# Kernel tuning notes

Measured on AMD Instinct MI355X. Metric: run time of the kernel, lower is better.

## Reference

```python
import jax, jax.numpy as jnp
import numpy as np

N_NODES = 100000
N_EDGES = 1600000
D = 128


def sage_conv(x, src, dst, W_l, b_l, W_r):
    # mean aggregation of neighbor features: messages flow src -> dst
    msgs = x[src]                                           # [E, D] gather
    agg = jax.ops.segment_sum(msgs, dst, num_segments=x.shape[0])  # [N, D]
    deg = jax.ops.segment_sum(jnp.ones((src.shape[0],), x.dtype), dst,
                              num_segments=x.shape[0])       # [N]
    agg = agg / jnp.maximum(deg, 1.0)[:, None]
    # PyG SAGEConv: lin_l(aggregated) + lin_r(root); bias lives in lin_l
    return agg @ W_l.T + b_l + x @ W_r.T


def setup_inputs() -> dict:
    key = jax.random.key(0)
    ks = jax.random.split(key, 8)
    s = 1.0 / np.sqrt(D)
    return {
        "x": jax.random.normal(ks[0], (N_NODES, D), dtype=jnp.float32),
        "edge_index": jax.random.randint(ks[1], (2, N_EDGES), 0, N_NODES, dtype=jnp.int64),
        "W1_l": jax.random.normal(ks[2], (D, D), dtype=jnp.float32) * s,
        "b1": jnp.zeros((D,), dtype=jnp.float32),
        "W1_r": jax.random.normal(ks[3], (D, D), dtype=jnp.float32) * s,
        "W2_l": jax.random.normal(ks[4], (D, D), dtype=jnp.float32) * s,
        "b2": jnp.zeros((D,), dtype=jnp.float32),
        "W2_r": jax.random.normal(ks[5], (D, D), dtype=jnp.float32) * s,
    }


def reference(x, edge_index, W1_l, b1, W1_r, W2_l, b2, W2_r):
    src, dst = edge_index[0], edge_index[1]
    h = jax.nn.relu(sage_conv(x, src, dst, W1_l, b1, W1_r))
    out = sage_conv(h, src, dst, W2_l, b2, W2_r)
    return out
```

## Files before the change

### kernel.cpp

```cpp
#include <hip/hip_runtime.h>
#include <cstdint>
#include <cstddef>

#define D 128

typedef unsigned short ushort_t;
typedef unsigned int uint_t;
typedef __attribute__((ext_vector_type(8))) short bf16x8;
typedef __attribute__((ext_vector_type(4))) float f32x4;

static __device__ __forceinline__ unsigned short f2bf(float f) {
    unsigned int u = __float_as_uint(f);
    u = (u + 0x7FFFu + ((u >> 16) & 1u)) >> 16;
    return (unsigned short)u;
}
static __device__ __forceinline__ float bf_lo(uint_t v) {
    return __uint_as_float(v << 16);
}
static __device__ __forceinline__ float bf_hi(uint_t v) {
    return __uint_as_float(v & 0xFFFF0000u);
}

static __device__ __forceinline__ void cast8(const float* __restrict__ s,
                                             ushort_t* __restrict__ d) {
    float4 a = *(const float4*)s;
    float4 b = *(const float4*)(s + 4);
    uint4 o;
    o.x = (uint_t)f2bf(a.x) | ((uint_t)f2bf(a.y) << 16);
    o.y = (uint_t)f2bf(a.z) | ((uint_t)f2bf(a.w) << 16);
    o.z = (uint_t)f2bf(b.x) | ((uint_t)f2bf(b.y) << 16);
    o.w = (uint_t)f2bf(b.z) | ((uint_t)f2bf(b.w) << 16);
    *(uint4*)d = o;
}


__global__ __launch_bounds__(256) void front_fused(
    const int* __restrict__ dst, int* __restrict__ bhist, int E, int EB,
    const float* __restrict__ x, ushort_t* __restrict__ xb, long nx, int CX,
    const float* __restrict__ W1l, const float* __restrict__ W1r,
    const float* __restrict__ W2l, const float* __restrict__ W2r,
    ushort_t* __restrict__ W1lb, ushort_t* __restrict__ W1rb,
    ushort_t* __restrict__ W2lb, ushort_t* __restrict__ W2rb,
    int* __restrict__ row_ptr, int N) {
    __shared__ int lh[512];
    int b = blockIdx.x, t = threadIdx.x;
    if (b == 0 && t == 0) row_ptr[N] = E;
    if (b < EB) {
        lh[t] = 0;
        lh[t + 256] = 0;
        __syncthreads();
        int base = b * 4096;
#pragma unroll
        for (int i = 0; i < 16; ++i) {
            int e = base + i * 256 + t;
            if (e < E) atomicAdd(&lh[dst[e] >> 8], 1);
        }
        __syncthreads();
        if (lh[t]) atomicAdd(&bhist[t], lh[t]);
        if (lh[t + 256]) atomicAdd(&bhist[t + 256], lh[t + 256]);
    } else if (b < EB + CX) {
        long i = ((long)(b - EB) * 256 + t) * 8;
        if (i < nx) cast8(x + i, xb + i);
    } else {
        int bb = b - EB - CX;
        int arr = bb >> 3;
        long i = ((long)(bb & 7) * 256 + t) * 8;
        const float* s = (arr == 0) ? W1l : (arr == 1) ? W1r
                       : (arr == 2) ? W2l : W2r;
        ushort_t* d = (arr == 0) ? W1lb : (arr == 1) ? W1rb
                    : (arr == 2) ? W2lb : W2rb;
        cast8(s + i, d + i);
    }
}


__global__ __launch_bounds__(256) void bkt_scatter2(const int* __restrict__ src,
                                                    const int* __restrict__ dst,
                                                    const int* __restrict__ bhist,
                                                    int* __restrict__ bcur,
                                                    int* __restrict__ ebuf, int E) {
    __shared__ int lh[512];
    __shared__ int lofs[512];
    __shared__ int gbs[512];
    __shared__ int tA[256];
    __shared__ int tB[256];
    __shared__ int sv[4096];
    __shared__ unsigned short sb[4096];
    int t = threadIdx.x;
    lh[t] = 0;
    lh[t + 256] = 0;
    __syncthreads();
    int base = blockIdx.x * 4096;
    unsigned pk[16];
#pragma unroll
    for (int i = 0; i < 16; ++i) {
        int e = base + i * 256 + t;
        unsigned p = 0xFFFFFFFFu;
        if (e < E) {
            int d = dst[e];
            int bkt = d >> 8;
            int r = atomicAdd(&lh[bkt], 1);
            p = ((unsigned)r << 17) | ((unsigned)bkt << 8) | (unsigned)(d & 255);
        }
        pk[i] = p;
    }
    __syncthreads();
    int a0 = lh[2 * t], a1 = lh[2 * t + 1];
    int g0 = bhist[2 * t], g1 = bhist[2 * t + 1];
    int ps = a0 + a1, gs = g0 + g1;
    tA[t] = ps;
    tB[t] = gs;
    __syncthreads();
    for (int off = 1; off < 256; off <<= 1) {
        int u1 = (t >= off) ? tA[t - off] : 0;
        int u2 = (t >= off) ? tB[t - off] : 0;
        __syncthreads();
        tA[t] += u1;
        tB[t] += u2;
        __syncthreads();
    }
    int lexb = tA[t] - ps;
    int gexb = tB[t] - gs;
    lofs[2 * t] = lexb;
    lofs[2 * t + 1] = lexb + a0;
    gbs[2 * t] = gexb;
    gbs[2 * t + 1] = gexb + g0;
    __syncthreads();
    if (a0) gbs[2 * t] += atomicAdd(&bcur[2 * t], a0);
    if (a1) gbs[2 * t + 1] += atomicAdd(&bcur[2 * t + 1], a1);
    __syncthreads();
#pragma unroll
    for (int i = 0; i < 16; ++i) {
        int e = base + i * 256 + t;
        if (e < E) {
            unsigned p = pk[i];
            int bkt = (p >> 8) & 511;
            int r = (int)(p >> 17);
            int pos = lofs[bkt] + r;
            sv[pos] = src[e] | ((int)(p & 255) << 20);
            sb[pos] = (unsigned short)bkt;
        }
    }
    __syncthreads();
    int cnt = min(E - base, 4096);
    for (int i = t; i < cnt; i += 256) {
        int b2 = sb[i];
        ebuf[gbs[b2] + (i - lofs[b2])] = sv[i];
    }
}

__global__ __launch_bounds__(256) void bkt_build2(const int* __restrict__ ebuf,
                                                  const int* __restrict__ bhist,
                                                  int* __restrict__ row_ptr,
                                                  int* __restrict__ csr, int N) {
    __shared__ int scn[512];
    __shared__ int tA[256];
    __shared__ int lcnt[256];
    __shared__ int lofs[256];
    __shared__ int lcur[256];
    int t = threadIdx.x;
    int b = blockIdx.x;
    int base = b << 8;
    int g0 = bhist[2 * t], g1 = bhist[2 * t + 1];
    int gs = g0 + g1;
    tA[t] = gs;
    __syncthreads();
    for (int off = 1; off < 256; off <<= 1) {
        int u = (t >= off) ? tA[t - off] : 0;
        __syncthreads();
        tA[t] += u;
        __syncthreads();
    }
    int gexb = tA[t] - gs;
    scn[2 * t] = gexb;
    scn[2 * t + 1] = gexb + g0;
    lcnt[t] = 0;
    __syncthreads();
    int ebeg = scn[b];
    int eend = ebeg + bhist[b];
    for (int e = ebeg + t; e < eend; e += 256)
        atomicAdd(&lcnt[((unsigned)ebuf[e]) >> 20], 1);
    __syncthreads();
    int v = lcnt[t];
    lofs[t] = v;
    __syncthreads();
    for (int off = 1; off < 256; off <<= 1) {
        int u = (t >= off) ? lofs[t - off] : 0;
        __syncthreads();
        lofs[t] += u;
        __syncthreads();
    }
    int ex = lofs[t] - v;
    __syncthreads();
    lofs[t] = ex;
    lcur[t] = 0;
    if (base + t < N) row_ptr[base + t] = ebeg + ex;
    __syncthreads();
    for (int e = ebeg + t; e < eend; e += 256) {
        int u = ebuf[e];
        int d = ((unsigned)u) >> 20;
        int r = atomicAdd(&lcur[d], 1);
        csr[ebeg + lofs[d] + r] = u & 0xFFFFF;
    }
}


static __device__ __forceinline__ void acc8(uint4 v, float a[8]) {
    a[0] += bf_lo(v.x); a[1] += bf_hi(v.x);
    a[2] += bf_lo(v.y); a[3] += bf_hi(v.y);
    a[4] += bf_lo(v.z); a[5] += bf_hi(v.z);
    a[6] += bf_lo(v.w); a[7] += bf_hi(v.w);
}

static __device__ __forceinline__ uint4 grow(const ushort_t* __restrict__ xin,
                                             int s, int l16) {
    unsigned off = ((unsigned)s << 8) | ((unsigned)l16 << 4);
    return *(const uint4*)((const char*)xin + off);
}

static __device__ __forceinline__ void agg_store(ushort_t* __restrict__ aggb,
                                                 int node, int l16,
                                                 const float a[8], int deg) {
    float inv = 1.0f / fmaxf((float)deg, 1.0f);
    uint4 o;
    o.x = (uint_t)f2bf(a[0] * inv) | ((uint_t)f2bf(a[1] * inv) << 16);
    o.y = (uint_t)f2bf(a[2] * inv) | ((uint_t)f2bf(a[3] * inv) << 16);
    o.z = (uint_t)f2bf(a[4] * inv) | ((uint_t)f2bf(a[5] * inv) << 16);
    o.w = (uint_t)f2bf(a[6] * inv) | ((uint_t)f2bf(a[7] * inv) << 16);
    unsigned off = ((unsigned)node << 8) | ((unsigned)l16 << 4);
    *(uint4*)((char*)aggb + off) = o;
}

__global__ __launch_bounds__(256) void agg_k2(const ushort_t* __restrict__ xin,
                                              const int* __restrict__ csr,
                                              const int* __restrict__ row_ptr,
                                              ushort_t* __restrict__ aggb, int N) {
    int wave = threadIdx.x >> 6;
    int lane = threadIdx.x & 63;
    int g = lane >> 4;
    int l16 = lane & 15;
    int p = blockIdx.x * 8 + wave * 2;
    if (p >= N) return;
    int node0 = p;
    int node1 = min(p + 1, N - 1);
    int b0 = row_ptr[node0];
    int deg0 = row_ptr[node0 + 1] - b0;
    int b1 = row_ptr[node1];
    int deg1 = row_ptr[node1 + 1] - b1;
    int d0 = min(deg0, 64), d1 = min(deg1, 64);
    int i0 = (deg0 > 0) ? csr[b0 + min(lane, deg0 - 1)] : 0;
    int i1 = (deg1 > 0) ? csr[b1 + min(lane, deg1 - 1)] : 0;
    int c0 = max(d0 - 1, 0), c1 = max(d1 - 1, 0);
    float a0[8] = {0.f, 0.f, 0.f, 0.f, 0.f, 0.f, 0.f, 0.f};
    float a1[8] = {0.f, 0.f, 0.f, 0.f, 0.f, 0.f, 0.f, 0.f};
    int mm = max(d0, d1);
    for (int e = 0; e < mm; e += 16) {
        bool do0 = (e < d0), do1 = (e < d1);
        uint4 v0[4], v1[4];
        if (do0) {
#pragma unroll
            for (int q = 0; q < 4; ++q) {
                int s = __shfl(i0, min(e + 4 * q + g, c0));
                v0[q] = grow(xin, s, l16);
            }
        }
        if (do1) {
#pragma unroll
            for (int q = 0; q < 4; ++q) {
                int s = __shfl(i1, min(e + 4 * q + g, c1));
                v1[q] = grow(xin, s, l16);
            }
        }
        if (do0) {
#pragma unroll
            for (int q = 0; q < 4; ++q)
                if (e + 4 * q + g < d0) acc8(v0[q], a0);
        }
        if (do1) {
#pragma unroll
            for (int q = 0; q < 4; ++q)
                if (e + 4 * q + g < d1) acc8(v1[q], a1);
        }
    }
    for (int e2 = 64; e2 < deg0; e2 += 4) {
        int s = csr[b0 + min(e2 + g, deg0 - 1)];
        uint4 v = grow(xin, s, l16);
        if (e2 + g < deg0) acc8(v, a0);
    }
    for (int e2 = 64; e2 < deg1; e2 += 4) {
        int s = csr[b1 + min(e2 + g, deg1 - 1)];
        uint4 v = grow(xin, s, l16);
        if (e2 + g < deg1) acc8(v, a1);
    }
#pragma unroll
    for (int i = 0; i < 8; ++i) {
        a0[i] += __shfl_xor(a0[i], 16);
        a1[i] += __shfl_xor(a1[i], 16);
        a0[i] += __shfl_xor(a0[i], 32);
        a1[i] += __shfl_xor(a1[i], 32);
    }
    if (g == 0) {
        agg_store(aggb, node0, l16, a0, deg0);
        agg_store(aggb, node1, l16, a1, deg1);
    }
}


__global__ __launch_bounds__(256) void gemm_mfma(const ushort_t* __restrict__ Aagg,
                                                 const ushort_t* __restrict__ Ax,
                                                 const ushort_t* __restrict__ Wl,
                                                 const ushort_t* __restrict__ Wr,
                                                 const float* __restrict__ bias,
                                                 ushort_t* __restrict__ out_bf,
                                                 float* __restrict__ out_f32,
                                                 int N, int relu_bf) {
    __shared__ ushort_t sA[128 * 32];
    __shared__ ushort_t sW[128 * 32];
    int tid = threadIdx.x;
    int wave = tid >> 6, lane = tid & 63;
    int quad = lane >> 4, l15 = lane & 15;
    int wm = wave & 1, wc = wave >> 1;
    int n0 = blockIdx.x * 128;
    int sr = tid >> 2;
    int sseg = (tid & 3) * 8;

    f32x4 acc[4][4];
#pragma unroll
    for (int mt = 0; mt < 4; ++mt)
#pragma unroll
        for (int nt = 0; nt < 4; ++nt) acc[mt][nt] = (f32x4){0.f, 0.f, 0.f, 0.f};

    int ga0 = min(n0 + sr, N - 1);
    int ga1 = min(n0 + sr + 64, N - 1);

#pragma unroll
    for (int c = 0; c < 8; ++c) {
        const ushort_t* Ab = (c < 4) ? Aagg : Ax;
        const ushort_t* Wb = (c < 4) ? Wl : Wr;
        int koff = (c & 3) * 32 + sseg;
        bf16x8 va0 = *(const bf16x8*)(Ab + (size_t)ga0 * D + koff);
        bf16x8 va1 = *(const bf16x8*)(Ab + (size_t)ga1 * D + koff);
        bf16x8 vw0 = *(const bf16x8*)(Wb + (size_t)sr * D + koff);
        bf16x8 vw1 = *(const bf16x8*)(Wb + (size_t)(sr + 64) * D + koff);
        __syncthreads();
        *(bf16x8*)&sA[sr * 32 + sseg] = va0;
        *(bf16x8*)&sA[(sr + 64) * 32 + sseg] = va1;
        *(bf16x8*)&sW[sr * 32 + sseg] = vw0;
        *(bf16x8*)&sW[(sr + 64) * 32 + sseg] = vw1;
        __syncthreads();

        bf16x8 af[4], wf[4];
#pragma unroll
        for (int mt = 0; mt < 4; ++mt)
            af[mt] = *(const bf16x8*)&sA[(wm * 64 + mt * 16 + l15) * 32 + quad * 8];
#pragma unroll
        for (int nt = 0; nt < 4; ++nt)
            wf[nt] = *(const bf16x8*)&sW[(wc * 64 + nt * 16 + l15) * 32 + quad * 8];
#pragma unroll
        for (int mt = 0; mt < 4; ++mt)
#pragma unroll
            for (int nt = 0; nt < 4; ++nt)
                acc[mt][nt] = __builtin_amdgcn_mfma_f32_16x16x32_bf16(
                    af[mt], wf[nt], acc[mt][nt], 0, 0, 0);
    }

#pragma unroll
    for (int mt = 0; mt < 4; ++mt) {
#pragma unroll
        for (int nt = 0; nt < 4; ++nt) {
            int col = wc * 64 + nt * 16 + l15;
            float bv = bias[col];
#pragma unroll
            for (int reg = 0; reg < 4; ++reg) {
                int row = n0 + wm * 64 + mt * 16 + quad * 4 + reg;
                if (row < N) {
                    float v = acc[mt][nt][reg] + bv;
                    if (relu_bf) {
                        v = fmaxf(v, 0.f);
                        out_bf[(size_t)row * D + col] = f2bf(v);
                    } else {
                        out_f32[(size_t)row * D + col] = v;
                    }
                }
            }
        }
    }
}


extern "C" void kernel_launch(void* const* d_in, const int* in_sizes, int n_in,
                              void* d_out, int out_size, void* d_ws, size_t ws_size,
                              hipStream_t stream) {
    const float* x   = (const float*)d_in[0];
    const int*   ei  = (const int*)d_in[1];
    const float* W1l = (const float*)d_in[2];
    const float* b1  = (const float*)d_in[3];
    const float* W1r = (const float*)d_in[4];
    const float* W2l = (const float*)d_in[5];
    const float* b2  = (const float*)d_in[6];
    const float* W2r = (const float*)d_in[7];
    float* out = (float*)d_out;

    int N = in_sizes[0] / D;
    int E = in_sizes[1] / 2;
    const int* src = ei;
    const int* dst = ei + E;

    char* ws = (char*)d_ws;
    size_t off = 0;
    auto take = [&](size_t bytes) -> char* {
        char* p = ws + off;
        off += (bytes + 255) & ~(size_t)255;
        return p;
    };
    int*      row_ptr = (int*)take((size_t)(N + 1) * sizeof(int));
    int*      bhist   = (int*)take((size_t)(512 + 512 + 513) * sizeof(int));
    int*      bcur    = bhist + 512;
    int*      ebuf    = (int*)take((size_t)E * sizeof(int));
    int*      csr     = (int*)take((size_t)E * sizeof(int));
    ushort_t* xb      = (ushort_t*)take((size_t)N * D * sizeof(ushort_t));
    ushort_t* hb      = (ushort_t*)take((size_t)N * D * sizeof(ushort_t));
    ushort_t* aggb    = (ushort_t*)take((size_t)N * D * sizeof(ushort_t));
    ushort_t* W1lb    = (ushort_t*)take((size_t)D * D * sizeof(ushort_t));
    ushort_t* W1rb    = (ushort_t*)take((size_t)D * D * sizeof(ushort_t));
    ushort_t* W2lb    = (ushort_t*)take((size_t)D * D * sizeof(ushort_t));
    ushort_t* W2rb    = (ushort_t*)take((size_t)D * D * sizeof(ushort_t));
    (void)ws_size;
    (void)n_in;
    (void)out_size;

    hipMemsetAsync(bhist, 0, 1024 * sizeof(int), stream);

    int NB = (N + 255) / 256;
    int EB = (E + 4095) / 4096;
    long nx = (long)N * D;
    int CX = (int)((nx / 8 + 255) / 256);

    front_fused<<<EB + CX + 32, 256, 0, stream>>>(
        dst, bhist, E, EB, x, xb, nx, CX,
        W1l, W1r, W2l, W2r, W1lb, W1rb, W2lb, W2rb, row_ptr, N);
    bkt_scatter2<<<EB, 256, 0, stream>>>(src, dst, bhist, bcur, ebuf, E);
    bkt_build2<<<NB, 256, 0, stream>>>(ebuf, bhist, row_ptr, csr, N);

    int ablocks = (N + 7) / 8;
    int gblocks = (N + 127) / 128;

    agg_k2<<<ablocks, 256, 0, stream>>>(xb, csr, row_ptr, aggb, N);
    gemm_mfma<<<gblocks, 256, 0, stream>>>(aggb, xb, W1lb, W1rb, b1, hb, nullptr, N, 1);

    agg_k2<<<ablocks, 256, 0, stream>>>(hb, csr, row_ptr, aggb, N);
    gemm_mfma<<<gblocks, 256, 0, stream>>>(aggb, hb, W2lb, W2rb, b2, nullptr, out, N, 0);
}
```

Measured before the change: 332.3 us.

## Use 128-node buckets, smaller scatter tiles, and 64-row GEMM tiles

The CSR build now uses 782 buckets of 128 destination nodes instead of 391 buckets of 256. The scatter kernel handles 1024 edges per block rather than 4096. The GEMM is retiled to 64 rows per block, with each wave owning 16 rows across all 128 columns. The aim is more blocks and better occupancy in the scatter, build and GEMM stages. The cost is more global atomics on the bucket counters and more reloading of W per row tile.

```diff
diff --git a/kernel.cpp b/kernel.cpp
--- a/kernel.cpp
+++ b/kernel.cpp
@@ -35,34 +35,36 @@
 
 
 __global__ __launch_bounds__(256) void front_fused(
-    const int* __restrict__ dst, int* __restrict__ bhist, int E, int EB,
+    const int* __restrict__ dst, int* __restrict__ bhist, int E, int EBH,
     const float* __restrict__ x, ushort_t* __restrict__ xb, long nx, int CX,
     const float* __restrict__ W1l, const float* __restrict__ W1r,
     const float* __restrict__ W2l, const float* __restrict__ W2r,
     ushort_t* __restrict__ W1lb, ushort_t* __restrict__ W1rb,
     ushort_t* __restrict__ W2lb, ushort_t* __restrict__ W2rb,
     int* __restrict__ row_ptr, int N) {
-    __shared__ int lh[512];
+    __shared__ int lh[1024];
     int b = blockIdx.x, t = threadIdx.x;
     if (b == 0 && t == 0) row_ptr[N] = E;
-    if (b < EB) {
-        lh[t] = 0;
-        lh[t + 256] = 0;
+    if (b < EBH) {
+        lh[t] = 0; lh[t + 256] = 0; lh[t + 512] = 0; lh[t + 768] = 0;
         __syncthreads();
         int base = b * 4096;
 #pragma unroll
         for (int i = 0; i < 16; ++i) {
             int e = base + i * 256 + t;
-            if (e < E) atomicAdd(&lh[dst[e] >> 8], 1);
-        }
-        __syncthreads();
-        if (lh[t]) atomicAdd(&bhist[t], lh[t]);
-        if (lh[t + 256]) atomicAdd(&bhist[t + 256], lh[t + 256]);
-    } else if (b < EB + CX) {
-        long i = ((long)(b - EB) * 256 + t) * 8;
+            if (e < E) atomicAdd(&lh[dst[e] >> 7], 1);
+        }
+        __syncthreads();
+#pragma unroll
+        for (int j = 0; j < 4; ++j) {
+            int v = lh[t + j * 256];
+            if (v) atomicAdd(&bhist[t + j * 256], v);
+        }
+    } else if (b < EBH + CX) {
+        long i = ((long)(b - EBH) * 256 + t) * 8;
         if (i < nx) cast8(x + i, xb + i);
     } else {
-        int bb = b - EB - CX;
+        int bb = b - EBH - CX;
         int arr = bb >> 3;
         long i = ((long)(bb & 7) * 256 + t) * 8;
         const float* s = (arr == 0) ? W1l : (arr == 1) ? W1r
@@ -74,41 +76,45 @@
 }
 
 
-__global__ __launch_bounds__(256) void bkt_scatter2(const int* __restrict__ src,
+__global__ __launch_bounds__(256) void bkt_scatter3(const int* __restrict__ src,
                                                     const int* __restrict__ dst,
                                                     const int* __restrict__ bhist,
                                                     int* __restrict__ bcur,
                                                     int* __restrict__ ebuf, int E) {
-    __shared__ int lh[512];
-    __shared__ int lofs[512];
-    __shared__ int gbs[512];
+    __shared__ int lh[1024];
+    __shared__ int lofs[1024];
+    __shared__ int gbs[1024];
     __shared__ int tA[256];
     __shared__ int tB[256];
-    __shared__ int sv[4096];
-    __shared__ unsigned short sb[4096];
+    __shared__ int sv[1024];
+    __shared__ unsigned short sb[1024];
     int t = threadIdx.x;
-    lh[t] = 0;
-    lh[t + 256] = 0;
-    __syncthreads();
-    int base = blockIdx.x * 4096;
-    unsigned pk[16];
-#pragma unroll
-    for (int i = 0; i < 16; ++i) {
+    lh[t] = 0; lh[t + 256] = 0; lh[t + 512] = 0; lh[t + 768] = 0;
+    __syncthreads();
+    int base = blockIdx.x * 1024;
+    unsigned pk[4];
+#pragma unroll
+    for (int i = 0; i < 4; ++i) {
         int e = base + i * 256 + t;
         unsigned p = 0xFFFFFFFFu;
         if (e < E) {
             int d = dst[e];
-            int bkt = d >> 8;
+            int bkt = d >> 7;
             int r = atomicAdd(&lh[bkt], 1);
-            p = ((unsigned)r << 17) | ((unsigned)bkt << 8) | (unsigned)(d & 255);
+            p = ((unsigned)r << 17) | ((unsigned)bkt << 7) | (unsigned)(d & 127);
         }
         pk[i] = p;
     }
     __syncthreads();
-    int a0 = lh[2 * t], a1 = lh[2 * t + 1];
-    int g0 = bhist[2 * t], g1 = bhist[2 * t + 1];
-    int ps = a0 + a1, gs = g0 + g1;
-    tA[t] = ps;
+    int la[4], ga[4];
+#pragma unroll
+    for (int j = 0; j < 4; ++j) {
+        la[j] = lh[4 * t + j];
+        ga[j] = bhist[4 * t + j];
+    }
+    int ls = la[0] + la[1] + la[2] + la[3];
+    int gs = ga[0] + ga[1] + ga[2] + ga[3];
+    tA[t] = ls;
     tB[t] = gs;
     __syncthreads();
     for (int off = 1; off < 256; off <<= 1) {
@@ -119,51 +125,57 @@
         tB[t] += u2;
         __syncthreads();
     }
-    int lexb = tA[t] - ps;
-    int gexb = tB[t] - gs;
-    lofs[2 * t] = lexb;
-    lofs[2 * t + 1] = lexb + a0;
-    gbs[2 * t] = gexb;
-    gbs[2 * t + 1] = gexb + g0;
-    __syncthreads();
-    if (a0) gbs[2 * t] += atomicAdd(&bcur[2 * t], a0);
-    if (a1) gbs[2 * t + 1] += atomicAdd(&bcur[2 * t + 1], a1);
-    __syncthreads();
-#pragma unroll
-    for (int i = 0; i < 16; ++i) {
+    int lrun = tA[t] - ls;
+    int grun = tB[t] - gs;
+#pragma unroll
+    for (int j = 0; j < 4; ++j) {
+        lofs[4 * t + j] = lrun;
+        gbs[4 * t + j] = grun;
+        lrun += la[j];
+        grun += ga[j];
+    }
+    __syncthreads();
+#pragma unroll
+    for (int j = 0; j < 4; ++j)
+        if (la[j]) gbs[4 * t + j] += atomicAdd(&bcur[4 * t + j], la[j]);
+    __syncthreads();
+#pragma unroll
+    for (int i = 0; i < 4; ++i) {
         int e = base + i * 256 + t;
         if (e < E) {
             unsigned p = pk[i];
-            int bkt = (p >> 8) & 511;
+            int bkt = (p >> 7) & 1023;
             int r = (int)(p >> 17);
             int pos = lofs[bkt] + r;
-            sv[pos] = src[e] | ((int)(p & 255) << 20);
+            sv[pos] = src[e] | ((int)(p & 127) << 20);
             sb[pos] = (unsigned short)bkt;
         }
     }
     __syncthreads();
-    int cnt = min(E - base, 4096);
+    int cnt = min(E - base, 1024);
     for (int i = t; i < cnt; i += 256) {
         int b2 = sb[i];
         ebuf[gbs[b2] + (i - lofs[b2])] = sv[i];
     }
 }
 
-__global__ __launch_bounds__(256) void bkt_build2(const int* __restrict__ ebuf,
+__global__ __launch_bounds__(256) void bkt_build3(const int* __restrict__ ebuf,
                                                   const int* __restrict__ bhist,
                                                   int* __restrict__ row_ptr,
                                                   int* __restrict__ csr, int N) {
-    __shared__ int scn[512];
+    __shared__ int scn[1024];
     __shared__ int tA[256];
-    __shared__ int lcnt[256];
-    __shared__ int lofs[256];
-    __shared__ int lcur[256];
+    __shared__ int lcnt[128];
+    __shared__ int lofs[128];
+    __shared__ int lcur[128];
     int t = threadIdx.x;
     int b = blockIdx.x;
-    int base = b << 8;
-    int g0 = bhist[2 * t], g1 = bhist[2 * t + 1];
-    int gs = g0 + g1;
+    int ga[4];
+#pragma unroll
+    for (int j = 0; j < 4; ++j) ga[j] = bhist[4 * t + j];
+    int gs = ga[0] + ga[1] + ga[2] + ga[3];
     tA[t] = gs;
+    if (t < 128) lcnt[t] = 0;
     __syncthreads();
     for (int off = 1; off < 256; off <<= 1) {
         int u = (t >= off) ? tA[t - off] : 0;
@@ -171,30 +183,38 @@
         tA[t] += u;
         __syncthreads();
     }
-    int gexb = tA[t] - gs;
-    scn[2 * t] = gexb;
-    scn[2 * t + 1] = gexb + g0;
-    lcnt[t] = 0;
+    int grun = tA[t] - gs;
+#pragma unroll
+    for (int j = 0; j < 4; ++j) {
+        scn[4 * t + j] = grun;
+        grun += ga[j];
+    }
     __syncthreads();
     int ebeg = scn[b];
     int eend = ebeg + bhist[b];
     for (int e = ebeg + t; e < eend; e += 256)
         atomicAdd(&lcnt[((unsigned)ebuf[e]) >> 20], 1);
     __syncthreads();
-    int v = lcnt[t];
-    lofs[t] = v;
-    __syncthreads();
-    for (int off = 1; off < 256; off <<= 1) {
-        int u = (t >= off) ? lofs[t - off] : 0;
-        __syncthreads();
-        lofs[t] += u;
-        __syncthreads();
-    }
-    int ex = lofs[t] - v;
-    __syncthreads();
-    lofs[t] = ex;
-    lcur[t] = 0;
-    if (base + t < N) row_ptr[base + t] = ebeg + ex;
+    int v = 0;
+    if (t < 128) {
+        v = lcnt[t];
+        lofs[t] = v;
+    }
+    __syncthreads();
+    for (int off = 1; off < 128; off <<= 1) {
+        int u = 0;
+        if (t < 128 && t >= off) u = lofs[t - off];
+        __syncthreads();
+        if (t < 128) lofs[t] += u;
+        __syncthreads();
+    }
+    if (t < 128) {
+        int ex = lofs[t] - v;
+        lofs[t] = ex;
+        lcur[t] = 0;
+        int node = (b << 7) + t;
+        if (node < N) row_ptr[node] = ebeg + ex;
+    }
     __syncthreads();
     for (int e = ebeg + t; e < eend; e += 256) {
         int u = ebuf[e];
@@ -306,81 +326,67 @@
 }
 
 
-__global__ __launch_bounds__(256) void gemm_mfma(const ushort_t* __restrict__ Aagg,
-                                                 const ushort_t* __restrict__ Ax,
-                                                 const ushort_t* __restrict__ Wl,
-                                                 const ushort_t* __restrict__ Wr,
-                                                 const float* __restrict__ bias,
-                                                 ushort_t* __restrict__ out_bf,
-                                                 float* __restrict__ out_f32,
-                                                 int N, int relu_bf) {
-    __shared__ ushort_t sA[128 * 32];
+__global__ __launch_bounds__(256) void gemm_mfma64(const ushort_t* __restrict__ Aagg,
+                                                   const ushort_t* __restrict__ Ax,
+                                                   const ushort_t* __restrict__ Wl,
+                                                   const ushort_t* __restrict__ Wr,
+                                                   const float* __restrict__ bias,
+                                                   ushort_t* __restrict__ out_bf,
+                                                   float* __restrict__ out_f32,
+                                                   int N, int relu_bf) {
+    __shared__ ushort_t sA[64 * 32];
     __shared__ ushort_t sW[128 * 32];
     int tid = threadIdx.x;
     int wave = tid >> 6, lane = tid & 63;
     int quad = lane >> 4, l15 = lane & 15;
-    int wm = wave & 1, wc = wave >> 1;
-    int n0 = blockIdx.x * 128;
+    int n0 = blockIdx.x * 64;
     int sr = tid >> 2;
     int sseg = (tid & 3) * 8;
 
-    f32x4 acc[4][4];
-#pragma unroll
-    for (int mt = 0; mt < 4; ++mt)
-#pragma unroll
-        for (int nt = 0; nt < 4; ++nt) acc[mt][nt] = (f32x4){0.f, 0.f, 0.f, 0.f};
-
-    int ga0 = min(n0 + sr, N - 1);
-    int ga1 = min(n0 + sr + 64, N - 1);
+    f32x4 acc[8];
+#pragma unroll
+    for (int nt = 0; nt < 8; ++nt) acc[nt] = (f32x4){0.f, 0.f, 0.f, 0.f};
+
+    int ga = min(n0 + sr, N - 1);
 
 #pragma unroll
     for (int c = 0; c < 8; ++c) {
         const ushort_t* Ab = (c < 4) ? Aagg : Ax;
         const ushort_t* Wb = (c < 4) ? Wl : Wr;
         int koff = (c & 3) * 32 + sseg;
-        bf16x8 va0 = *(const bf16x8*)(Ab + (size_t)ga0 * D + koff);
-        bf16x8 va1 = *(const bf16x8*)(Ab + (size_t)ga1 * D + koff);
+        bf16x8 va = *(const bf16x8*)(Ab + (size_t)ga * D + koff);
         bf16x8 vw0 = *(const bf16x8*)(Wb + (size_t)sr * D + koff);
         bf16x8 vw1 = *(const bf16x8*)(Wb + (size_t)(sr + 64) * D + koff);
         __syncthreads();
-        *(bf16x8*)&sA[sr * 32 + sseg] = va0;
-        *(bf16x8*)&sA[(sr + 64) * 32 + sseg] = va1;
+        *(bf16x8*)&sA[sr * 32 + sseg] = va;
         *(bf16x8*)&sW[sr * 32 + sseg] = vw0;
         *(bf16x8*)&sW[(sr + 64) * 32 + sseg] = vw1;
         __syncthreads();
 
-        bf16x8 af[4], wf[4];
-#pragma unroll
-        for (int mt = 0; mt < 4; ++mt)
-            af[mt] = *(const bf16x8*)&sA[(wm * 64 + mt * 16 + l15) * 32 + quad * 8];
-#pragma unroll
-        for (int nt = 0; nt < 4; ++nt)
-            wf[nt] = *(const bf16x8*)&sW[(wc * 64 + nt * 16 + l15) * 32 + quad * 8];
-#pragma unroll
-        for (int mt = 0; mt < 4; ++mt)
-#pragma unroll
-            for (int nt = 0; nt < 4; ++nt)
-                acc[mt][nt] = __builtin_amdgcn_mfma_f32_16x16x32_bf16(
-                    af[mt], wf[nt], acc[mt][nt], 0, 0, 0);
-    }
-
-#pragma unroll
-    for (int mt = 0; mt < 4; ++mt) {
-#pragma unroll
-        for (int nt = 0; nt < 4; ++nt) {
-            int col = wc * 64 + nt * 16 + l15;
-            float bv = bias[col];
-#pragma unroll
-            for (int reg = 0; reg < 4; ++reg) {
-                int row = n0 + wm * 64 + mt * 16 + quad * 4 + reg;
-                if (row < N) {
-                    float v = acc[mt][nt][reg] + bv;
-                    if (relu_bf) {
-                        v = fmaxf(v, 0.f);
-                        out_bf[(size_t)row * D + col] = f2bf(v);
-                    } else {
-                        out_f32[(size_t)row * D + col] = v;
-                    }
+        bf16x8 af = *(const bf16x8*)&sA[(wave * 16 + l15) * 32 + quad * 8];
+        bf16x8 wf[8];
+#pragma unroll
+        for (int nt = 0; nt < 8; ++nt)
+            wf[nt] = *(const bf16x8*)&sW[(nt * 16 + l15) * 32 + quad * 8];
+#pragma unroll
+        for (int nt = 0; nt < 8; ++nt)
+            acc[nt] = __builtin_amdgcn_mfma_f32_16x16x32_bf16(af, wf[nt], acc[nt], 0, 0, 0);
+    }
+
+#pragma unroll
+    for (int nt = 0; nt < 8; ++nt) {
+        int col = nt * 16 + l15;
+        float bv = bias[col];
+#pragma unroll
+        for (int reg = 0; reg < 4; ++reg) {
+            int row = n0 + wave * 16 + quad * 4 + reg;
+            if (row < N) {
+                float v = acc[nt][reg] + bv;
+                if (relu_bf) {
+                    v = fmaxf(v, 0.f);
+                    out_bf[(size_t)row * D + col] = f2bf(v);
+                } else {
+                    out_f32[(size_t)row * D + col] = v;
                 }
             }
         }
@@ -414,8 +420,8 @@
         return p;
     };
     int*      row_ptr = (int*)take((size_t)(N + 1) * sizeof(int));
-    int*      bhist   = (int*)take((size_t)(512 + 512 + 513) * sizeof(int));
-    int*      bcur    = bhist + 512;
+    int*      bhist   = (int*)take((size_t)2048 * sizeof(int));
+    int*      bcur    = bhist + 1024;
     int*      ebuf    = (int*)take((size_t)E * sizeof(int));
     int*      csr     = (int*)take((size_t)E * sizeof(int));
     ushort_t* xb      = (ushort_t*)take((size_t)N * D * sizeof(ushort_t));
@@ -429,25 +435,26 @@
     (void)n_in;
     (void)out_size;
 
-    hipMemsetAsync(bhist, 0, 1024 * sizeof(int), stream);
-
-    int NB = (N + 255) / 256;
-    int EB = (E + 4095) / 4096;
+    hipMemsetAsync(bhist, 0, 2048 * sizeof(int), stream);
+
+    int EBH = (E + 4095) / 4096;
+    int EBS = (E + 1023) / 1024;
+    int NBB = (N + 127) / 128;
     long nx = (long)N * D;
     int CX = (int)((nx / 8 + 255) / 256);
 
-    front_fused<<<EB + CX + 32, 256, 0, stream>>>(
-        dst, bhist, E, EB, x, xb, nx, CX,
+    front_fused<<<EBH + CX + 32, 256, 0, stream>>>(
+        dst, bhist, E, EBH, x, xb, nx, CX,
         W1l, W1r, W2l, W2r, W1lb, W1rb, W2lb, W2rb, row_ptr, N);
-    bkt_scatter2<<<EB, 256, 0, stream>>>(src, dst, bhist, bcur, ebuf, E);
-    bkt_build2<<<NB, 256, 0, stream>>>(ebuf, bhist, row_ptr, csr, N);
+    bkt_scatter3<<<EBS, 256, 0, stream>>>(src, dst, bhist, bcur, ebuf, E);
+    bkt_build3<<<NBB, 256, 0, stream>>>(ebuf, bhist, row_ptr, csr, N);
 
     int ablocks = (N + 7) / 8;
-    int gblocks = (N + 127) / 128;
+    int gblocks = (N + 63) / 64;
 
     agg_k2<<<ablocks, 256, 0, stream>>>(xb, csr, row_ptr, aggb, N);
-    gemm_mfma<<<gblocks, 256, 0, stream>>>(aggb, xb, W1lb, W1rb, b1, hb, nullptr, N, 1);
+    gemm_mfma64<<<gblocks, 256, 0, stream>>>(aggb, xb, W1lb, W1rb, b1, hb, nullptr, N, 1);
 
     agg_k2<<<ablocks, 256, 0, stream>>>(hb, csr, row_ptr, aggb, N);
-    gemm_mfma<<<gblocks, 256, 0, stream>>>(aggb, hb, W2lb, W2rb, b2, nullptr, out, N, 0);
-}
+    gemm_mfma64<<<gblocks, 256, 0, stream>>>(aggb, hb, W2lb, W2rb, b2, nullptr, out, N, 0);
+}
```

After: 428.4 us. 1.29x slower.

## Replace atomic bucket counters with per-block histogram and column prefix scan

Applied to the files above, without the earlier changes.

Each histogram block now writes its own 512-bucket counts to a per-block table instead of atomically adding into a global histogram. A new column-scan kernel computes per-block exclusive offsets and bucket totals, so the scatter kernel reads deterministic offsets instead of using atomic cursors. This drops the memset and the global atomics and makes edge order deterministic, at the cost of an extra kernel launch and a strided transposed read of the block histogram table. EB is 391 here, so it fits within the scan's 512 limit.

```diff
diff --git a/kernel.cpp b/kernel.cpp
--- a/kernel.cpp
+++ b/kernel.cpp
@@ -35,7 +35,7 @@
 
 
 __global__ __launch_bounds__(256) void front_fused(
-    const int* __restrict__ dst, int* __restrict__ bhist, int E, int EB,
+    const int* __restrict__ dst, int* __restrict__ blkhist, int E, int EB,
     const float* __restrict__ x, ushort_t* __restrict__ xb, long nx, int CX,
     const float* __restrict__ W1l, const float* __restrict__ W1r,
     const float* __restrict__ W2l, const float* __restrict__ W2r,
@@ -56,8 +56,8 @@
             if (e < E) atomicAdd(&lh[dst[e] >> 8], 1);
         }
         __syncthreads();
-        if (lh[t]) atomicAdd(&bhist[t], lh[t]);
-        if (lh[t + 256]) atomicAdd(&bhist[t + 256], lh[t + 256]);
+        blkhist[(size_t)b * 512 + t] = lh[t];
+        blkhist[(size_t)b * 512 + 256 + t] = lh[t + 256];
     } else if (b < EB + CX) {
         long i = ((long)(b - EB) * 256 + t) * 8;
         if (i < nx) cast8(x + i, xb + i);
@@ -74,10 +74,36 @@
 }
 
 
-__global__ __launch_bounds__(256) void bkt_scatter2(const int* __restrict__ src,
+__global__ __launch_bounds__(256) void colscan(int* __restrict__ blkhist,
+                                               int* __restrict__ bhist, int EB) {
+    __shared__ int arr[512];
+    __shared__ int tA[256];
+    int k = blockIdx.x;
+    int t = threadIdx.x;
+    arr[t] = (t < EB) ? blkhist[(size_t)t * 512 + k] : 0;
+    arr[t + 256] = (t + 256 < EB) ? blkhist[(size_t)(t + 256) * 512 + k] : 0;
+    __syncthreads();
+    int a0 = arr[2 * t], a1 = arr[2 * t + 1];
+    int ps = a0 + a1;
+    tA[t] = ps;
+    __syncthreads();
+    for (int off = 1; off < 256; off <<= 1) {
+        int u = (t >= off) ? tA[t - off] : 0;
+        __syncthreads();
+        tA[t] += u;
+        __syncthreads();
+    }
+    int exb = tA[t] - ps;
+    if (2 * t < EB) blkhist[(size_t)(2 * t) * 512 + k] = exb;
+    if (2 * t + 1 < EB) blkhist[(size_t)(2 * t + 1) * 512 + k] = exb + a0;
+    if (t == 255) bhist[k] = tA[255];
+}
+
+
+__global__ __launch_bounds__(256) void bkt_scatter4(const int* __restrict__ src,
                                                     const int* __restrict__ dst,
                                                     const int* __restrict__ bhist,
-                                                    int* __restrict__ bcur,
+                                                    const int* __restrict__ blkhist,
                                                     int* __restrict__ ebuf, int E) {
     __shared__ int lh[512];
     __shared__ int lofs[512];
@@ -87,10 +113,11 @@
     __shared__ int sv[4096];
     __shared__ unsigned short sb[4096];
     int t = threadIdx.x;
+    int blk = blockIdx.x;
     lh[t] = 0;
     lh[t + 256] = 0;
     __syncthreads();
-    int base = blockIdx.x * 4096;
+    int base = blk * 4096;
     unsigned pk[16];
 #pragma unroll
     for (int i = 0; i < 16; ++i) {
@@ -123,11 +150,8 @@
     int gexb = tB[t] - gs;
     lofs[2 * t] = lexb;
     lofs[2 * t + 1] = lexb + a0;
-    gbs[2 * t] = gexb;
-    gbs[2 * t + 1] = gexb + g0;
-    __syncthreads();
-    if (a0) gbs[2 * t] += atomicAdd(&bcur[2 * t], a0);
-    if (a1) gbs[2 * t + 1] += atomicAdd(&bcur[2 * t + 1], a1);
+    gbs[2 * t] = gexb + blkhist[(size_t)blk * 512 + 2 * t];
+    gbs[2 * t + 1] = gexb + g0 + blkhist[(size_t)blk * 512 + 2 * t + 1];
     __syncthreads();
 #pragma unroll
     for (int i = 0; i < 16; ++i) {
@@ -148,6 +172,7 @@
         ebuf[gbs[b2] + (i - lofs[b2])] = sv[i];
     }
 }
+
 
 __global__ __launch_bounds__(256) void bkt_build2(const int* __restrict__ ebuf,
                                                   const int* __restrict__ bhist,
@@ -406,6 +431,11 @@
     const int* src = ei;
     const int* dst = ei + E;
 
+    int EB = (E + 4095) / 4096;
+    int NB = (N + 255) / 256;
+    long nx = (long)N * D;
+    int CX = (int)((nx / 8 + 255) / 256);
+
     char* ws = (char*)d_ws;
     size_t off = 0;
     auto take = [&](size_t bytes) -> char* {
@@ -414,8 +444,8 @@
         return p;
     };
     int*      row_ptr = (int*)take((size_t)(N + 1) * sizeof(int));
-    int*      bhist   = (int*)take((size_t)(512 + 512 + 513) * sizeof(int));
-    int*      bcur    = bhist + 512;
+    int*      bhist   = (int*)take((size_t)512 * sizeof(int));
+    int*      blkhist = (int*)take((size_t)EB * 512 * sizeof(int));
     int*      ebuf    = (int*)take((size_t)E * sizeof(int));
     int*      csr     = (int*)take((size_t)E * sizeof(int));
     ushort_t* xb      = (ushort_t*)take((size_t)N * D * sizeof(ushort_t));
@@ -429,17 +459,11 @@
     (void)n_in;
     (void)out_size;
 
-    hipMemsetAsync(bhist, 0, 1024 * sizeof(int), stream);
-
-    int NB = (N + 255) / 256;
-    int EB = (E + 4095) / 4096;
-    long nx = (long)N * D;
-    int CX = (int)((nx / 8 + 255) / 256);
-
     front_fused<<<EB + CX + 32, 256, 0, stream>>>(
-        dst, bhist, E, EB, x, xb, nx, CX,
+        dst, blkhist, E, EB, x, xb, nx, CX,
         W1l, W1r, W2l, W2r, W1lb, W1rb, W2lb, W2rb, row_ptr, N);
-    bkt_scatter2<<<EB, 256, 0, stream>>>(src, dst, bhist, bcur, ebuf, E);
+    colscan<<<512, 256, 0, stream>>>(blkhist, bhist, EB);
+    bkt_scatter4<<<EB, 256, 0, stream>>>(src, dst, bhist, blkhist, ebuf, E);
     bkt_build2<<<NB, 256, 0, stream>>>(ebuf, bhist, row_ptr, csr, N);
 
     int ablocks = (N + 7) / 8;
```

Result: faster. 321.6 us (-3.2%).
